# Optimization experiments

Hardware: AMD Instinct MI355X
Metric: run time of the kernel (lower is better)

## Reference

```python
import jax, jax.numpy as jnp
import numpy as np

BLOCK = 8
C = 64


def setup_inputs() -> dict:
    key = jax.random.key(0)
    k = jax.random.split(key, 6)
    B, H, W = 4, 512, 512
    x = jax.random.normal(k[0], (B, C, H, W), jnp.float32)
    # per-channel 8x8 transform matrices (torch.randn init)
    tw = jax.random.normal(k[1], (C, BLOCK, BLOCK), jnp.float32)
    s = 1.0 / np.sqrt(C).astype(np.float32)
    w1 = jax.random.normal(k[2], (C, C), jnp.float32) * s  # 1x1 conv weight [out,in]
    b1 = jax.random.normal(k[3], (C,), jnp.float32) * s
    w2 = jax.random.normal(k[4], (C, C), jnp.float32) * s
    b2 = jax.random.normal(k[5], (C,), jnp.float32) * s
    return {"x": x, "tw": tw, "w1": w1, "b1": b1, "w2": w2, "b2": b2}


def reference(x, tw, w1, b1, w2, b2):
    B, Cc, H, W = x.shape
    bs = BLOCK
    nh, nw = H // bs, W // bs
    # extract 8x8 blocks: [b,c,nh,nw,i,j]
    p = x.reshape(B, Cc, nh, bs, nw, bs).transpose(0, 1, 2, 4, 3, 5)
    # per-channel T @ P @ T^T : out[p,q] = T[p,i] P[i,j] T[q,j]
    t = jnp.einsum('cpi,bcnmij,cqj->bcnmpq', tw, p, tw)
    # fold blocks back to image
    y = t.transpose(0, 1, 2, 4, 3, 5).reshape(B, Cc, H, W)
    # quantization gate: 1x1 conv -> relu -> 1x1 conv -> sigmoid
    g = jnp.einsum('oc,bchw->bohw', w1, y) + b1[None, :, None, None]
    g = jax.nn.relu(g)
    g = jnp.einsum('oc,bchw->bohw', w2, g) + b2[None, :, None, None]
    g = jax.nn.sigmoid(g)
    return y * g
```

## Files before the change

### kernel.cpp

```cpp
#include <hip/hip_runtime.h>

typedef float f4 __attribute__((ext_vector_type(4)));
typedef __attribute__((ext_vector_type(4))) float f32x4;
typedef _Float16 h8 __attribute__((ext_vector_type(8)));

__device__ __forceinline__ void gload_lds16(const float* g, float* l) {
    __builtin_amdgcn_global_load_lds(
        (const __attribute__((address_space(1))) void*)g,
        (__attribute__((address_space(3))) void*)l, 16, 0, 0);
}

__global__ __launch_bounds__(256, 2)
void avif_final(const float* __restrict__ x, const float* __restrict__ twm,
                const float* __restrict__ w1, const float* __restrict__ b1,
                const float* __restrict__ w2, const float* __restrict__ b2,
                float* __restrict__ out)
{
    __shared__ float xs[8192];
    __shared__ ushort ysf[128][64];
    __shared__ ushort hsf[128][64];
    __shared__ float ts[4096];

    const int t = threadIdx.x;
    const int bid = blockIdx.x;
    const int wc  = bid >> 8;
    const int rem = bid & 255;
    const int hb  = rem & 63;
    const int b   = rem >> 6;

    const int wv = t >> 6, lane = t & 63;
    const int li = lane & 15, lg = lane >> 4, l7 = li & 7;
    const int lb3 = (li >> 3) << 2;

    const float* xslab = x + (((size_t)(b * 64)) * 512 + (size_t)hb * 8) * 512 + wc * 16;
    const float* gp[8];
#pragma unroll
    for (int j = 0; j < 8; ++j) {
        const int G = j * 256 + t;
        const int c = G >> 5;
        const int v = (G & 31) ^ (c & 7);
        const int r = v >> 2, qg = v & 3;
        gp[j] = xslab + (size_t)c * 262144 + r * 512 + qg * 4;
    }
    float* lbase = &xs[wv * 256];

#pragma unroll
    for (int j = 0; j < 4; ++j) {
        const int g = j * 256 + t;
        const int c = g >> 4, s = g & 15;
        const int kg = s ^ (c & 15);
        *(f4*)&ts[c * 64 + s * 4] = *(const f4*)(twm + c * 64 + kg * 4);
    }

    h8 w1f[2], w2f[2];
    {
        const float* p1 = w1 + (16 * wv + li) * 64 + lg * 8;
        const float* p2 = w2 + (16 * wv + li) * 64 + lg * 8;
#pragma unroll
        for (int kk = 0; kk < 2; ++kk) {
            f4 a = *(const f4*)(p1 + kk * 32);
            f4 d = *(const f4*)(p1 + kk * 32 + 4);
            h8 f;
#pragma unroll
            for (int q = 0; q < 4; ++q) { f[q] = (_Float16)a[q]; f[4 + q] = (_Float16)d[q]; }
            w1f[kk] = f;
            a = *(const f4*)(p2 + kk * 32);
            d = *(const f4*)(p2 + kk * 32 + 4);
#pragma unroll
            for (int q = 0; q < 4; ++q) { f[q] = (_Float16)a[q]; f[4 + q] = (_Float16)d[q]; }
            w2f[kk] = f;
        }
    }
    const int o0 = 16 * wv + 4 * lg;
    const f4 b1v = *(const f4*)(b1 + o0);
    const float b2s = b2[16 * wv + li];
    const int sg0 = ((lg       ^ l7 ^ lb3) << 3);
    const int sg1 = (((4 + lg) ^ l7 ^ lb3) << 3);
    const int go  = o0 >> 3, co = 4 * (lg & 1);
    const int ch  = 16 * wv + li;
    const int cgE = ch >> 3, c7E = li & 7;

    const int pid = t >> 1, h2 = t & 1;
    const int c   = pid & 63, blk = pid >> 6, Q0 = 4 * h2;
    const int tc  = c * 64, c15 = c & 15;
    const int sc = c * 128, swc = c & 7;
    const int cg = c >> 3, c7 = c & 7;

#pragma unroll
    for (int j = 0; j < 8; ++j) gload_lds16(gp[j], lbase + j * 1024);
    asm volatile("s_waitcnt vmcnt(0)" ::: "memory");
    __syncthreads();

    for (int tile = 0; tile < 16; ++tile) {
        const int wt = 2 * tile + wc;

        {
            float M[8][4];
            {
                f4 Ph[8];
#pragma unroll
                for (int i = 0; i < 8; ++i)
                    Ph[i] = *(const f4*)&xs[sc + ((i * 4 + blk * 2) ^ swc) * 4];
#pragma unroll
                for (int qq = 0; qq < 4; ++qq) {
                    f4 Th = *(const f4*)&ts[tc + ((2 * (Q0 + qq)) ^ c15) * 4];
#pragma unroll
                    for (int i = 0; i < 8; ++i) {
                        float s = Ph[i][0] * Th[0];
                        s = fmaf(Ph[i][1], Th[1], s);
                        s = fmaf(Ph[i][2], Th[2], s);
                        s = fmaf(Ph[i][3], Th[3], s);
                        M[i][qq] = s;
                    }
                }
#pragma unroll
                for (int i = 0; i < 8; ++i)
                    Ph[i] = *(const f4*)&xs[sc + ((i * 4 + blk * 2 + 1) ^ swc) * 4];
#pragma unroll
                for (int qq = 0; qq < 4; ++qq) {
                    f4 Th = *(const f4*)&ts[tc + ((2 * (Q0 + qq) + 1) ^ c15) * 4];
#pragma unroll
                    for (int i = 0; i < 8; ++i) {
                        float s = M[i][qq];
                        s = fmaf(Ph[i][0], Th[0], s);
                        s = fmaf(Ph[i][1], Th[1], s);
                        s = fmaf(Ph[i][2], Th[2], s);
                        s = fmaf(Ph[i][3], Th[3], s);
                        M[i][qq] = s;
                    }
                }
            }
#pragma unroll
            for (int p = 0; p < 8; ++p) {
                f4 a = *(const f4*)&ts[tc + ((2 * p)     ^ c15) * 4];
                f4 d = *(const f4*)&ts[tc + ((2 * p + 1) ^ c15) * 4];
                const int px0 = p * 16 + blk * 8;
#pragma unroll
                for (int qq = 0; qq < 4; ++qq) {
                    const int q = Q0 + qq;
                    float s = a[0] * M[0][qq];
                    s = fmaf(a[1], M[1][qq], s);
                    s = fmaf(a[2], M[2][qq], s);
                    s = fmaf(a[3], M[3][qq], s);
                    s = fmaf(d[0], M[4][qq], s);
                    s = fmaf(d[1], M[5][qq], s);
                    s = fmaf(d[2], M[6][qq], s);
                    s = fmaf(d[3], M[7][qq], s);
                    const int idx = ((cg ^ q ^ (blk << 2)) << 3) | c7;
                    *(_Float16*)&ysf[px0 + q][idx] = (_Float16)s;
                }
            }
        }
        __syncthreads();

        if (tile < 15) {
#pragma unroll
            for (int j = 0; j < 8; ++j)
                gload_lds16(gp[j] + (tile + 1) * 32, lbase + j * 1024);
        }

        f32x4 acc[8];
#pragma unroll
        for (int j = 0; j < 8; ++j) acc[j] = (f32x4){0.f, 0.f, 0.f, 0.f};
#pragma unroll
        for (int j = 0; j < 8; ++j) {
            const int row = 16 * j + li;
            h8 bh0 = *(const h8*)&ysf[row][sg0];
            h8 bh1 = *(const h8*)&ysf[row][sg1];
            acc[j] = __builtin_amdgcn_mfma_f32_16x16x32_f16(w1f[0], bh0, acc[j], 0, 0, 0);
            acc[j] = __builtin_amdgcn_mfma_f32_16x16x32_f16(w1f[1], bh1, acc[j], 0, 0, 0);
        }
#pragma unroll
        for (int j = 0; j < 8; ++j) {
            const int px = 16 * j + li;
            const int idx = ((go ^ l7 ^ lb3) << 3) + co;
            union { _Float16 h[2]; unsigned u; } p01, p23;
            p01.h[0] = (_Float16)fmaxf(acc[j][0] + b1v[0], 0.f);
            p01.h[1] = (_Float16)fmaxf(acc[j][1] + b1v[1], 0.f);
            p23.h[0] = (_Float16)fmaxf(acc[j][2] + b1v[2], 0.f);
            p23.h[1] = (_Float16)fmaxf(acc[j][3] + b1v[3], 0.f);
            *(unsigned*)&hsf[px][idx]     = p01.u;
            *(unsigned*)&hsf[px][idx + 2] = p23.u;
        }
        __syncthreads();

#pragma unroll
        for (int j = 0; j < 8; ++j) acc[j] = (f32x4){0.f, 0.f, 0.f, 0.f};
#pragma unroll
        for (int j = 0; j < 8; ++j) {
            const int row = 16 * j + li;
            h8 ah0 = *(const h8*)&hsf[row][sg0];
            h8 ah1 = *(const h8*)&hsf[row][sg1];
            acc[j] = __builtin_amdgcn_mfma_f32_16x16x32_f16(ah0, w2f[0], acc[j], 0, 0, 0);
            acc[j] = __builtin_amdgcn_mfma_f32_16x16x32_f16(ah1, w2f[1], acc[j], 0, 0, 0);
        }
        float* oB = out + ((size_t)(b * 64) + ch) * 262144
                    + (size_t)(hb * 8) * 512 + wt * 16 + 4 * lg;
#pragma unroll
        for (int j = 0; j < 8; ++j) {
            f4 r;
#pragma unroll
            for (int r4 = 0; r4 < 4; ++r4) {
                const int pc = 4 * lg + r4;
                const int px = 16 * j + pc;
                const int idx = ((cgE ^ (pc & 7) ^ (((pc >> 3) & 1) << 2)) << 3) | c7E;
                float yv = (float)(*(const _Float16*)&ysf[px][idx]);
                float z = acc[j][r4] + b2s;
                float g = __builtin_amdgcn_rcpf(1.f + __expf(-z));
                r[r4] = yv * g;
            }
            *(f4*)(oB + (size_t)j * 512) = r;
        }
        asm volatile("s_waitcnt vmcnt(0)" ::: "memory");
        __syncthreads();
    }
}

extern "C" void kernel_launch(void* const* d_in, const int* in_sizes, int n_in,
                              void* d_out, int out_size, void* d_ws, size_t ws_size,
                              hipStream_t stream) {
    (void)in_sizes; (void)n_in; (void)out_size; (void)d_ws; (void)ws_size;
    const float* x   = (const float*)d_in[0];
    const float* twm = (const float*)d_in[1];
    const float* w1  = (const float*)d_in[2];
    const float* b1  = (const float*)d_in[3];
    const float* w2  = (const float*)d_in[4];
    const float* b2  = (const float*)d_in[5];
    float* out = (float*)d_out;

    avif_final<<<dim3(512), dim3(256), 0, stream>>>(x, twm, w1, b1, w2, b2, out);
}
```

Baseline: 168.2 us.

## Split fused kernel into block-transform and gating kernels via fp16 workspace

Breaks the single fused kernel into two launches. The first computes the per-channel 8x8 transform and writes fp16 tiles to a workspace. The second runs the two 1x1 conv MFMAs and the sigmoid gate, double-buffering workspace tiles into LDS. The aim is higher occupancy and more parallelism than the 512-block fused kernel, but it adds an extra 128MB round trip through global memory plus a second launch. If the workspace is too small it falls back to the old kernel.

```diff
diff --git a/kernel.cpp b/kernel.cpp
--- a/kernel.cpp
+++ b/kernel.cpp
@@ -4,10 +4,227 @@
 typedef __attribute__((ext_vector_type(4))) float f32x4;
 typedef _Float16 h8 __attribute__((ext_vector_type(8)));
 
-__device__ __forceinline__ void gload_lds16(const float* g, float* l) {
+__device__ __forceinline__ void gload_lds16(const void* g, void* l) {
     __builtin_amdgcn_global_load_lds(
         (const __attribute__((address_space(1))) void*)g,
         (__attribute__((address_space(3))) void*)l, 16, 0, 0);
+}
+
+#define BAR_LG()  do { asm volatile("s_waitcnt lgkmcnt(0)" ::: "memory"); \
+    __builtin_amdgcn_s_barrier(); asm volatile("" ::: "memory"); } while (0)
+#define BAR_VM8() do { asm volatile("s_waitcnt vmcnt(8) lgkmcnt(0)" ::: "memory"); \
+    __builtin_amdgcn_s_barrier(); asm volatile("" ::: "memory"); } while (0)
+#define BAR_VM0() do { asm volatile("s_waitcnt vmcnt(0) lgkmcnt(0)" ::: "memory"); \
+    __builtin_amdgcn_s_barrier(); asm volatile("" ::: "memory"); } while (0)
+
+__global__ __launch_bounds__(256, 3)
+void avif_k1(const float* __restrict__ x, const float* __restrict__ twm,
+             ushort* __restrict__ wsy)
+{
+    __shared__ ushort ysf[128][64];
+
+    const int t = threadIdx.x;
+    const int bid = blockIdx.x;
+    const int b3 = (bid >> 3) & 1;
+    const int u  = ((bid >> 4) << 3) | (bid & 7);
+    const int wt = ((u & 15) << 1) | b3;
+    const int hb = (u >> 4) & 63;
+    const int b  = u >> 10;
+
+    {
+        const int pid = t >> 1, h2 = t & 1;
+        const int c = pid & 63, blk = pid >> 6, Q0 = 4 * h2;
+        const float* xB = x + ((size_t)(b * 64 + c) * 512 + hb * 8) * 512
+                            + wt * 16 + blk * 8;
+        const float* tB = twm + c * 64;
+
+        float M[8][4];
+        {
+            f4 Ph[8];
+#pragma unroll
+            for (int i = 0; i < 8; ++i) Ph[i] = *(const f4*)(xB + i * 512);
+#pragma unroll
+            for (int qq = 0; qq < 4; ++qq) {
+                f4 Th = *(const f4*)(tB + (Q0 + qq) * 8);
+#pragma unroll
+                for (int i = 0; i < 8; ++i) {
+                    float s = Ph[i][0] * Th[0];
+                    s = fmaf(Ph[i][1], Th[1], s);
+                    s = fmaf(Ph[i][2], Th[2], s);
+                    s = fmaf(Ph[i][3], Th[3], s);
+                    M[i][qq] = s;
+                }
+            }
+#pragma unroll
+            for (int i = 0; i < 8; ++i) Ph[i] = *(const f4*)(xB + i * 512 + 4);
+#pragma unroll
+            for (int qq = 0; qq < 4; ++qq) {
+                f4 Th = *(const f4*)(tB + (Q0 + qq) * 8 + 4);
+#pragma unroll
+                for (int i = 0; i < 8; ++i) {
+                    float s = M[i][qq];
+                    s = fmaf(Ph[i][0], Th[0], s);
+                    s = fmaf(Ph[i][1], Th[1], s);
+                    s = fmaf(Ph[i][2], Th[2], s);
+                    s = fmaf(Ph[i][3], Th[3], s);
+                    M[i][qq] = s;
+                }
+            }
+        }
+        const int cg = c >> 3, c7 = c & 7;
+#pragma unroll
+        for (int p = 0; p < 8; ++p) {
+            f4 a = *(const f4*)(tB + p * 8);
+            f4 d = *(const f4*)(tB + p * 8 + 4);
+            const int px0 = p * 16 + blk * 8;
+#pragma unroll
+            for (int qq = 0; qq < 4; ++qq) {
+                const int q = Q0 + qq;
+                float s = a[0] * M[0][qq];
+                s = fmaf(a[1], M[1][qq], s);
+                s = fmaf(a[2], M[2][qq], s);
+                s = fmaf(a[3], M[3][qq], s);
+                s = fmaf(d[0], M[4][qq], s);
+                s = fmaf(d[1], M[5][qq], s);
+                s = fmaf(d[2], M[6][qq], s);
+                s = fmaf(d[3], M[7][qq], s);
+                const int idx = ((cg ^ q ^ (blk << 2)) << 3) | c7;
+                *(_Float16*)&ysf[px0 + q][idx] = (_Float16)s;
+            }
+        }
+    }
+    __syncthreads();
+
+    ushort* wdst = wsy + (size_t)(((b * 64 + hb) * 32) + wt) * 8192;
+    const ushort* ysl = &ysf[0][0];
+#pragma unroll
+    for (int j = 0; j < 4; ++j)
+        *(f4*)(wdst + t * 8 + j * 2048) = *(const f4*)(ysl + t * 8 + j * 2048);
+}
+
+__global__ __launch_bounds__(256, 3)
+void avif_k2(const ushort* __restrict__ wsy, const float* __restrict__ w1,
+             const float* __restrict__ b1, const float* __restrict__ w2,
+             const float* __restrict__ b2, float* __restrict__ out)
+{
+    __shared__ ushort yst[2][128][64];
+    __shared__ ushort hsf[128][64];
+
+    const int t = threadIdx.x;
+    const int bid = blockIdx.x;
+    const int wseg = bid & 3;
+    const int hb = (bid >> 2) & 63;
+    const int b  = bid >> 8;
+
+    const int wv = t >> 6, lane = t & 63;
+    const int li = lane & 15, lg = lane >> 4, l7 = li & 7;
+    const int lb3 = (li >> 3) << 2;
+
+    h8 w1f[2], w2f[2];
+    {
+        const float* p1 = w1 + (16 * wv + li) * 64 + lg * 8;
+        const float* p2 = w2 + (16 * wv + li) * 64 + lg * 8;
+#pragma unroll
+        for (int kk = 0; kk < 2; ++kk) {
+            f4 a = *(const f4*)(p1 + kk * 32);
+            f4 d = *(const f4*)(p1 + kk * 32 + 4);
+            h8 f;
+#pragma unroll
+            for (int q = 0; q < 4; ++q) { f[q] = (_Float16)a[q]; f[4 + q] = (_Float16)d[q]; }
+            w1f[kk] = f;
+            a = *(const f4*)(p2 + kk * 32);
+            d = *(const f4*)(p2 + kk * 32 + 4);
+#pragma unroll
+            for (int q = 0; q < 4; ++q) { f[q] = (_Float16)a[q]; f[4 + q] = (_Float16)d[q]; }
+            w2f[kk] = f;
+        }
+    }
+    const int o0 = 16 * wv + 4 * lg;
+    const f4 b1v = *(const f4*)(b1 + o0);
+    const float b2s = b2[16 * wv + li];
+    const int sg0 = ((lg       ^ l7 ^ lb3) << 3);
+    const int sg1 = (((4 + lg) ^ l7 ^ lb3) << 3);
+    const int go  = o0 >> 3, co = 4 * (lg & 1);
+    const int ch  = 16 * wv + li;
+    const int cgE = ch >> 3, c7E = li & 7;
+
+    const ushort* wsrc = wsy + (size_t)((b * 64 + hb) * 32 + wseg * 8) * 8192;
+    ushort* dst0 = &yst[0][0][0];
+    ushort* dst1 = &yst[1][0][0];
+    const int doff = wv * 512;
+
+#pragma unroll
+    for (int j = 0; j < 4; ++j)
+        gload_lds16(wsrc + (size_t)(j * 256 + t) * 8, dst0 + doff + j * 2048);
+    BAR_VM0();
+
+#pragma unroll 1
+    for (int k = 0; k < 8; ++k) {
+        const int buf = k & 1;
+        const int wt = wseg * 8 + k;
+
+        if (k < 7) {
+            const ushort* src = wsrc + (size_t)(k + 1) * 8192;
+            ushort* db = buf ? dst0 : dst1;
+#pragma unroll
+            for (int j = 0; j < 4; ++j)
+                gload_lds16(src + (size_t)(j * 256 + t) * 8, db + doff + j * 2048);
+        }
+
+        f32x4 acc[8];
+#pragma unroll
+        for (int j = 0; j < 8; ++j) acc[j] = (f32x4){0.f, 0.f, 0.f, 0.f};
+#pragma unroll
+        for (int j = 0; j < 8; ++j) {
+            const int row = 16 * j + li;
+            h8 bh0 = *(const h8*)&yst[buf][row][sg0];
+            h8 bh1 = *(const h8*)&yst[buf][row][sg1];
+            acc[j] = __builtin_amdgcn_mfma_f32_16x16x32_f16(w1f[0], bh0, acc[j], 0, 0, 0);
+            acc[j] = __builtin_amdgcn_mfma_f32_16x16x32_f16(w1f[1], bh1, acc[j], 0, 0, 0);
+        }
+#pragma unroll
+        for (int j = 0; j < 8; ++j) {
+            const int px = 16 * j + li;
+            const int idx = ((go ^ l7 ^ lb3) << 3) + co;
+            union { _Float16 h[2]; unsigned u; } p01, p23;
+            p01.h[0] = (_Float16)fmaxf(acc[j][0] + b1v[0], 0.f);
+            p01.h[1] = (_Float16)fmaxf(acc[j][1] + b1v[1], 0.f);
+            p23.h[0] = (_Float16)fmaxf(acc[j][2] + b1v[2], 0.f);
+            p23.h[1] = (_Float16)fmaxf(acc[j][3] + b1v[3], 0.f);
+            *(unsigned*)&hsf[px][idx]     = p01.u;
+            *(unsigned*)&hsf[px][idx + 2] = p23.u;
+        }
+        BAR_LG();
+
+#pragma unroll
+        for (int j = 0; j < 8; ++j) acc[j] = (f32x4){0.f, 0.f, 0.f, 0.f};
+#pragma unroll
+        for (int j = 0; j < 8; ++j) {
+            const int row = 16 * j + li;
+            h8 ah0 = *(const h8*)&hsf[row][sg0];
+            h8 ah1 = *(const h8*)&hsf[row][sg1];
+            acc[j] = __builtin_amdgcn_mfma_f32_16x16x32_f16(ah0, w2f[0], acc[j], 0, 0, 0);
+            acc[j] = __builtin_amdgcn_mfma_f32_16x16x32_f16(ah1, w2f[1], acc[j], 0, 0, 0);
+        }
+        float* oB = out + ((size_t)(b * 64) + ch) * 262144
+                    + (size_t)(hb * 8) * 512 + wt * 16 + 4 * lg;
+#pragma unroll
+        for (int j = 0; j < 8; ++j) {
+            f4 r;
+#pragma unroll
+            for (int r4 = 0; r4 < 4; ++r4) {
+                const int pc = 4 * lg + r4;
+                const int px = 16 * j + pc;
+                const int idx = ((cgE ^ (pc & 7) ^ (((pc >> 3) & 1) << 2)) << 3) | c7E;
+                float yv = (float)(*(const _Float16*)&yst[buf][px][idx]);
+                float z = acc[j][r4] + b2s;
+                float g = __builtin_amdgcn_rcpf(1.f + __expf(-z));
+                r[r4] = yv * g;
+            }
+            *(f4*)(oB + (size_t)j * 512) = r;
+        }
+        if (k < 7) BAR_VM8();
+    }
 }
 
 __global__ __launch_bounds__(256, 2)
@@ -93,7 +310,6 @@
 
     for (int tile = 0; tile < 16; ++tile) {
         const int wt = 2 * tile + wc;
-
         {
             float M[8][4];
             {
@@ -219,7 +435,7 @@
 extern "C" void kernel_launch(void* const* d_in, const int* in_sizes, int n_in,
                               void* d_out, int out_size, void* d_ws, size_t ws_size,
                               hipStream_t stream) {
-    (void)in_sizes; (void)n_in; (void)out_size; (void)d_ws; (void)ws_size;
+    (void)in_sizes; (void)n_in; (void)out_size;
     const float* x   = (const float*)d_in[0];
     const float* twm = (const float*)d_in[1];
     const float* w1  = (const float*)d_in[2];
@@ -228,5 +444,12 @@
     const float* b2  = (const float*)d_in[5];
     float* out = (float*)d_out;
 
-    avif_final<<<dim3(512), dim3(256), 0, stream>>>(x, twm, w1, b1, w2, b2, out);
+    const size_t need = (size_t)4 * 64 * 512 * 512 * 2;
+    if (ws_size >= need) {
+        ushort* wsy = (ushort*)d_ws;
+        avif_k1<<<dim3(4 * 64 * 32), dim3(256), 0, stream>>>(x, twm, wsy);
+        avif_k2<<<dim3(1024), dim3(256), 0, stream>>>(wsy, w1, b1, w2, b2, out);
+    } else {
+        avif_final<<<dim3(512), dim3(256), 0, stream>>>(x, twm, w1, b1, w2, b2, out);
+    }
 }
```

New measurement: 273.0 us. 1.62x slower.
